# Kernel optimization log

Hardware: AMD Instinct MI355X
Metric: run time of the kernel (lower is better)

The kernel has to match this reference:

```python
import jax, jax.numpy as jnp
import numpy as np

B, T, C, H = 8, 2048, 1024, 16
D = C // H  # head dim


def setup_inputs() -> dict:
    key = jax.random.key(0)
    k1, k2, k3 = jax.random.split(key, 3)
    x = jax.random.normal(k1, (B, T, C), dtype=jnp.float32)
    attention_mask = jnp.ones((B, 1, T), dtype=jnp.int32)
    w_attn = jax.random.normal(k2, (C, 3 * C), dtype=jnp.float32) * 0.02
    b_attn = jnp.zeros((3 * C,), dtype=jnp.float32)
    w_proj = jax.random.normal(k3, (C, C), dtype=jnp.float32) * (0.02 / np.sqrt(2 * 12))
    b_proj = jnp.zeros((C,), dtype=jnp.float32)
    return {"x": x, "attention_mask": attention_mask, "w_attn": w_attn,
            "b_attn": b_attn, "w_proj": w_proj, "b_proj": b_proj}


def reference(x, attention_mask, w_attn, b_attn, w_proj, b_proj):
    Bx, Tx, Cx = x.shape
    qkv = x @ w_attn + b_attn                      # [B,T,3C]
    q, k, v = jnp.split(qkv, 3, axis=2)
    def heads(t):
        return t.reshape(Bx, Tx, H, D).transpose(0, 2, 1, 3)  # [B,H,T,D]
    q, k, v = heads(q), heads(k), heads(v)
    phi_q = jax.nn.elu(q) + 1.0
    phi_k = jax.nn.elu(k) + 1.0
    valid_keys = jnp.any(attention_mask > 0, axis=1).astype(x.dtype)  # [B,T]
    mask = valid_keys[:, None, :, None]            # [B,1,T,1]
    phi_k = phi_k * mask
    v = v * mask
    kv = jnp.einsum('bhtd,bhtf->bhdf', phi_k, v)   # [B,H,D,D]
    k_sum = jnp.sum(phi_k, axis=2, keepdims=True)  # [B,H,1,D]
    numerator = jnp.einsum('bhtd,bhdf->bhtf', phi_q, kv)       # [B,H,T,D]
    denominator = jnp.einsum('bhtd,bhrd->bhtr', phi_q, k_sum)  # [B,H,T,1]
    denominator = jnp.maximum(denominator, 1e-08)
    y = numerator / denominator
    y = y.transpose(0, 2, 1, 3).reshape(Bx, Tx, Cx)
    return y @ w_proj + b_proj
```

## Files before the change

### kernel.cpp

```cpp
#include <hip/hip_runtime.h>

#define Tdim 2048

typedef __attribute__((ext_vector_type(8))) short bf16x8;
typedef __attribute__((ext_vector_type(4))) float f32x4;
typedef __attribute__((ext_vector_type(4))) short short4v;

#define GLOBAL_U32(p) ((const __attribute__((address_space(1))) unsigned int*)(p))
#define LDS_U32(p)    ((__attribute__((address_space(3))) unsigned int*)(p))

#define BARRIER() do { asm volatile("" ::: "memory"); \
                       __builtin_amdgcn_s_barrier(); \
                       asm volatile("" ::: "memory"); } while (0)

__device__ __forceinline__ float phi_f(float x) {
    return x > 0.f ? (x + 1.f) : __expf(x);
}
__device__ __forceinline__ short f2bf(float f) {
    unsigned u = __float_as_uint(f);
    u += 0x7fffu + ((u >> 16) & 1u);
    return (short)(u >> 16);
}
__device__ __forceinline__ float bf2f(short h) {
    return __uint_as_float(((unsigned)(unsigned short)h) << 16);
}


__device__ __forceinline__ void w_tile_body(
    const float* __restrict__ W, int N,
    short* __restrict__ Thi, short* __restrict__ Tlo, int bid)
{
    const int tile = bid * 4 + (threadIdx.x >> 6);
    const int nt = tile >> 5;
    const int kt = tile & 31;
    const int lane = threadIdx.x & 63;
    const int n = nt * 16 + (lane & 15);
    const int k = kt * 32 + (lane >> 4) * 8;
    const float* wp = W + (size_t)k * N + n;
    bf16x8 h, l;
#pragma unroll
    for (int j = 0; j < 8; ++j) {
        const float v = wp[(size_t)j * N];
        const short hh = f2bf(v);
        h[j] = hh;
        l[j] = f2bf(v - bf2f(hh));
    }
    const size_t off = (size_t)tile * 512 + lane * 8;
    *(bf16x8*)(Thi + off) = h;
    *(bf16x8*)(Tlo + off) = l;
}

__global__ __launch_bounds__(256) void prep_kernel(
    const float* __restrict__ X, short* __restrict__ Hi, short* __restrict__ Lo,
    const float* __restrict__ Wa, short* __restrict__ WaHi, short* __restrict__ WaLo,
    const float* __restrict__ Wp, short* __restrict__ WpHi, short* __restrict__ WpLo)
{
    const int bid = blockIdx.x;
    if (bid < 8192) {
        const int rt = bid >> 3;
        const int cb = bid & 7;
        const int t = threadIdx.x;
        const int rl = t >> 4;
        const int cc = t & 15;
        const float* xp = X + ((size_t)rt * 16 + rl) * 1024 + cb * 128 + cc * 8;
        const float4 a = *(const float4*)xp;
        const float4 b = *(const float4*)(xp + 4);
        float v[8] = {a.x, a.y, a.z, a.w, b.x, b.y, b.z, b.w};
        bf16x8 h, l;
#pragma unroll
        for (int j = 0; j < 8; ++j) {
            const short hh = f2bf(v[j]);
            h[j] = hh;
            l[j] = f2bf(v[j] - bf2f(hh));
        }
        const int kt = cb * 4 + (cc >> 2);
        const int slot = ((cc & 3) << 4) | rl;
        const size_t off = ((size_t)rt * 32 + kt) * 512 + slot * 8;
        *(bf16x8*)(Hi + off) = h;
        *(bf16x8*)(Lo + off) = l;
    } else if (bid < 8192 + 1536) {
        w_tile_body(Wa, 3072, WaHi, WaLo, bid - 8192);
    } else {
        w_tile_body(Wp, 1024, WpHi, WpLo, bid - 9728);
    }
}

template<int AMODE>
__global__ __launch_bounds__(512, 2) void gemm3_kernel(
    const short* __restrict__ Ahi, const short* __restrict__ Alo, int lda,
    const short* __restrict__ BThi, const short* __restrict__ BTlo,
    const float* __restrict__ bias, float* __restrict__ C,
    int K, int ldc)
{
    __shared__ short smem[65536];
    const int tid = threadIdx.x;
    const int lane = tid & 63;
    const int wid = tid >> 6;
    const int bx = blockIdx.x, by = blockIdx.y;
    const int wm = wid >> 2, wn = wid & 3;

    const size_t tilestep = (size_t)(K >> 5) * 512;

    const int sel = wid >> 1, half = wid & 1;
    const bool is_a_wave = (wid < 4);
    const short* gptr;
    if (sel >= 2) {
        const short* gb = (sel == 2) ? BThi : BTlo;
        gptr = gb + (size_t)(bx * 16 + half * 8) * tilestep + lane * 8;
    } else if (AMODE == 0) {
        const short* gb = (sel == 0) ? Ahi : Alo;
        gptr = gb + (size_t)(by * 16 + half * 8) * tilestep + lane * 8;
    } else {
        gptr = Ahi + (size_t)((by * 16 + half * 8) * 16) * 6144 + 2048 + lane * 8;
    }
    short* lw = smem + sel * 8192 + half * 4096;

    f32x4 acc[8][4];
#pragma unroll
    for (int i = 0; i < 8; ++i)
#pragma unroll
        for (int j = 0; j < 4; ++j) acc[i][j] = (f32x4){0.f, 0.f, 0.f, 0.f};

    auto stage = [&](int buf, int k0) {
        short* lb = lw + buf * 32768;
        if (AMODE == 0 || sel >= 2) {
            const short* g = gptr + (size_t)(k0 >> 5) * 512;
#pragma unroll
            for (int c = 0; c < 8; ++c)
                __builtin_amdgcn_global_load_lds(
                    GLOBAL_U32(g + (size_t)c * tilestep),
                    LDS_U32(lb + c * 512), 16, 0, 0);
        } else {
            const size_t koff = (size_t)(k0 >> 6) * 6144
                              + (size_t)((((k0 >> 5) & 1) << 1) | sel) * 512;
            const short* g = gptr + koff;
#pragma unroll
            for (int c = 0; c < 8; ++c)
                __builtin_amdgcn_global_load_lds(
                    GLOBAL_U32(g + (size_t)(c * 16) * 6144),
                    LDS_U32(lb + c * 512), 16, 0, 0);
        }
    };

    stage(0, 0);
    __syncthreads();

    const int fo = lane * 8;
    int cur = 0;
    for (int k0 = 0; k0 < K; k0 += 32) {
        const short* bp = smem + cur * 32768;
        const int k0n = (k0 + 32 < K) ? (k0 + 32) : 0;

        if (!is_a_wave) stage(cur ^ 1, k0n);
        bf16x8 bh[4], bl[4];
#pragma unroll
        for (int j = 0; j < 4; ++j) {
            bh[j] = *(const bf16x8*)(bp + 16384 + (wn * 4 + j) * 512 + fo);
            bl[j] = *(const bf16x8*)(bp + 24576 + (wn * 4 + j) * 512 + fo);
        }
        if (is_a_wave) asm volatile("s_waitcnt vmcnt(0)" ::: "memory");
        BARRIER();

        if (is_a_wave) stage(cur ^ 1, k0n);
        __builtin_amdgcn_s_setprio(1);
#pragma unroll
        for (int i = 0; i < 8; ++i) {
            const bf16x8 ah = *(const bf16x8*)(bp + (wm * 8 + i) * 512 + fo);
            const bf16x8 al = *(const bf16x8*)(bp + 8192 + (wm * 8 + i) * 512 + fo);
#pragma unroll
            for (int j = 0; j < 4; ++j) {
                acc[i][j] = __builtin_amdgcn_mfma_f32_16x16x32_bf16(ah, bh[j], acc[i][j], 0, 0, 0);
                acc[i][j] = __builtin_amdgcn_mfma_f32_16x16x32_bf16(al, bh[j], acc[i][j], 0, 0, 0);
                acc[i][j] = __builtin_amdgcn_mfma_f32_16x16x32_bf16(ah, bl[j], acc[i][j], 0, 0, 0);
            }
        }
        __builtin_amdgcn_s_setprio(0);
        if (!is_a_wave) asm volatile("s_waitcnt vmcnt(0)" ::: "memory");
        BARRIER();
        cur ^= 1;
    }

    const int fr = lane & 15, fq = lane >> 4;
#pragma unroll
    for (int i = 0; i < 8; ++i) {
        const size_t row0 = (size_t)by * 256 + wm * 128 + i * 16 + fq * 4;
#pragma unroll
        for (int j = 0; j < 4; ++j) {
            const int col = bx * 256 + wn * 64 + j * 16 + fr;
            const float bv = bias[col];
            float* cp = C + row0 * (size_t)ldc + col;
#pragma unroll
            for (int r = 0; r < 4; ++r)
                cp[(size_t)r * ldc] = acc[i][j][r] + bv;
        }
    }
}

__global__ __launch_bounds__(256) void kv_part_kernel(
    const float* __restrict__ qkv, const int* __restrict__ attn,
    float* __restrict__ kvpart, float* __restrict__ kspart)
{
    __shared__ float ks[32][64];
    __shared__ float vs[32][64];

    const int chunk = blockIdx.x;
    const int bh = blockIdx.y;
    const int b = bh >> 4;
    const int h = bh & 15;
    const int tid = threadIdx.x;
    const int tx = tid & 15;
    const int ty = tid >> 4;
    const int l_t = tid >> 4;
    const int l_d = (tid & 15) << 2;

    const float* kb = qkv + (size_t)b * Tdim * 3072 + 1024 + h * 64;
    const float* vb = qkv + (size_t)b * Tdim * 3072 + 2048 + h * 64;
    const int* am = attn + b * Tdim;

    float acc[4][4];
#pragma unroll
    for (int i = 0; i < 4; ++i)
#pragma unroll
        for (int j = 0; j < 4; ++j) acc[i][j] = 0.f;
    float ksl = 0.f;

    for (int t0 = chunk * 256; t0 < (chunk + 1) * 256; t0 += 32) {
        __syncthreads();
#pragma unroll
        for (int rr = 0; rr < 2; ++rr) {
            const int t = l_t + rr * 16;
            const int gt = t0 + t;
            const float m = (am[gt] > 0) ? 1.f : 0.f;
            const float4 k4 = *(const float4*)(kb + (size_t)gt * 3072 + l_d);
            const float4 v4 = *(const float4*)(vb + (size_t)gt * 3072 + l_d);
            float4 kp, vp;
            kp.x = phi_f(k4.x) * m; kp.y = phi_f(k4.y) * m;
            kp.z = phi_f(k4.z) * m; kp.w = phi_f(k4.w) * m;
            vp.x = v4.x * m; vp.y = v4.y * m; vp.z = v4.z * m; vp.w = v4.w * m;
            *(float4*)&ks[t][l_d] = kp;
            *(float4*)&vs[t][l_d] = vp;
        }
        __syncthreads();
#pragma unroll
        for (int t = 0; t < 32; ++t) {
            float kr[4], vr[4];
            *(float4*)kr = *(const float4*)&ks[t][ty * 4];
            *(float4*)vr = *(const float4*)&vs[t][tx * 4];
#pragma unroll
            for (int i = 0; i < 4; ++i)
#pragma unroll
                for (int j = 0; j < 4; ++j)
                    acc[i][j] = fmaf(kr[i], vr[j], acc[i][j]);
        }
        if (tid < 64) {
#pragma unroll
            for (int t = 0; t < 32; ++t) ksl += ks[t][tid];
        }
    }

    float* ko = kvpart + ((size_t)bh * 8 + chunk) * 4096;
#pragma unroll
    for (int i = 0; i < 4; ++i) {
        float4 o;
        o.x = acc[i][0]; o.y = acc[i][1]; o.z = acc[i][2]; o.w = acc[i][3];
        *(float4*)(ko + (ty * 4 + i) * 64 + tx * 4) = o;
    }
    if (tid < 64) kspart[((size_t)bh * 8 + chunk) * 64 + tid] = ksl;
}

__global__ __launch_bounds__(256) void kv_reduce_kernel(
    const float* __restrict__ kvpart, const float* __restrict__ kspart,
    short* __restrict__ kvT, float* __restrict__ ksum)
{
    __shared__ float kvs[64][68];
    const int bh = blockIdx.x;
    const int tid = threadIdx.x;
    const float4* p = (const float4*)(kvpart + (size_t)bh * 8 * 4096);
    float4 s0 = {0,0,0,0}, s1 = {0,0,0,0}, s2 = {0,0,0,0}, s3 = {0,0,0,0};
#pragma unroll
    for (int c = 0; c < 8; ++c) {
        const int base = c * 1024;
        float4 a = p[base + tid], b = p[base + 256 + tid],
               cc = p[base + 512 + tid], d = p[base + 768 + tid];
        s0.x += a.x; s0.y += a.y; s0.z += a.z; s0.w += a.w;
        s1.x += b.x; s1.y += b.y; s1.z += b.z; s1.w += b.w;
        s2.x += cc.x; s2.y += cc.y; s2.z += cc.z; s2.w += cc.w;
        s3.x += d.x; s3.y += d.y; s3.z += d.z; s3.w += d.w;
    }
    const int d0 = tid >> 4, f0 = (tid & 15) * 4;
    *(float4*)&kvs[d0 +  0][f0] = s0;
    *(float4*)&kvs[d0 + 16][f0] = s1;
    *(float4*)&kvs[d0 + 32][f0] = s2;
    *(float4*)&kvs[d0 + 48][f0] = s3;
    __syncthreads();

    short* kvb = kvT + (size_t)bh * 8192;
#pragma unroll
    for (int pp = 0; pp < 2; ++pp) {
        const int sid = tid * 2 + pp;
        const int tt = sid >> 6;
        const int L = sid & 63;
        const int nt = tt >> 1, kt = tt & 1;
        const int f = nt * 16 + (L & 15);
        const int dd = kt * 32 + (L >> 4) * 8;
        bf16x8 h, l;
#pragma unroll
        for (int e = 0; e < 8; ++e) {
            const float v = kvs[dd + e][f];
            const short hh = f2bf(v);
            h[e] = hh;
            l[e] = f2bf(v - bf2f(hh));
        }
        *(bf16x8*)(kvb + tt * 512 + L * 8) = h;
        *(bf16x8*)(kvb + 4096 + tt * 512 + L * 8) = l;
    }
    if (tid < 64) {
        float ss = 0.f;
#pragma unroll
        for (int c = 0; c < 8; ++c) ss += kspart[((size_t)bh * 8 + c) * 64 + tid];
        ksum[bh * 64 + tid] = ss;
    }
}

__global__ __launch_bounds__(256) void attn_y_kernel(
    float* __restrict__ qkv, const short* __restrict__ kvT,
    const float* __restrict__ ksumin)
{
    __shared__ short kvs[8192];
    __shared__ float den_s[4][16];

    const int bh = blockIdx.y;
    const int b = bh >> 4;
    const int hh = bh & 15;
    const int t0 = blockIdx.x * 64;
    const int tid = threadIdx.x;
    const int lane = tid & 63;
    const int wid = tid >> 6;

    {
        const short* src = kvT + (size_t)bh * 8192 + (wid * 4) * 512 + lane * 8;
        short* dst = kvs + (wid * 4) * 512;
#pragma unroll
        for (int t = 0; t < 4; ++t)
            __builtin_amdgcn_global_load_lds(
                GLOBAL_U32(src + t * 512), LDS_U32(dst + t * 512), 16, 0, 0);
    }

    const int grow = b * Tdim + t0 + wid * 16 + (lane & 15);
    const int kc = (lane >> 4) * 8;
    const float* qp = qkv + (size_t)grow * 3072 + hh * 64 + kc;
    const float* kp = ksumin + bh * 64 + kc;
    bf16x8 qh[2], ql[2];
    float den = 0.f;
#pragma unroll
    for (int ks = 0; ks < 2; ++ks) {
        const float4 a = *(const float4*)(qp + ks * 32);
        const float4 c = *(const float4*)(qp + ks * 32 + 4);
        const float4 u = *(const float4*)(kp + ks * 32);
        const float4 w = *(const float4*)(kp + ks * 32 + 4);
        float qv[8] = {a.x, a.y, a.z, a.w, c.x, c.y, c.z, c.w};
        float sv[8] = {u.x, u.y, u.z, u.w, w.x, w.y, w.z, w.w};
#pragma unroll
        for (int e = 0; e < 8; ++e) {
            const float ph = phi_f(qv[e]);
            den = fmaf(ph, sv[e], den);
            const short hi = f2bf(ph);
            qh[ks][e] = hi;
            ql[ks][e] = f2bf(ph - bf2f(hi));
        }
    }
    den += __shfl_xor(den, 16);
    den += __shfl_xor(den, 32);
    if ((lane >> 4) == 0) den_s[wid][lane & 15] = den;
    __syncthreads();

    f32x4 acc[4];
#pragma unroll
    for (int j = 0; j < 4; ++j) acc[j] = (f32x4){0.f, 0.f, 0.f, 0.f};
#pragma unroll
    for (int j = 0; j < 4; ++j) {
#pragma unroll
        for (int ks = 0; ks < 2; ++ks) {
            const short* tb = kvs + (j * 2 + ks) * 512 + lane * 8;
            const bf16x8 ahf = *(const bf16x8*)tb;
            const bf16x8 alf = *(const bf16x8*)(tb + 4096);
            acc[j] = __builtin_amdgcn_mfma_f32_16x16x32_bf16(ahf, qh[ks], acc[j], 0, 0, 0);
            acc[j] = __builtin_amdgcn_mfma_f32_16x16x32_bf16(alf, qh[ks], acc[j], 0, 0, 0);
            acc[j] = __builtin_amdgcn_mfma_f32_16x16x32_bf16(ahf, ql[ks], acc[j], 0, 0, 0);
        }
    }

    const float dinv = 1.f / fmaxf(den_s[wid][lane & 15], 1e-8f);

    short* yb = (short*)qkv;
    const int RT = ((b * Tdim + t0) >> 4) + wid;
    const size_t rowbase = (size_t)(RT * 16 + hh) * 6144 + 2048;
    const int fq = lane >> 4;
    const int trow = lane & 15;
#pragma unroll
    for (int j = 0; j < 4; ++j) {
        short4v hv, lv;
#pragma unroll
        for (int r = 0; r < 4; ++r) {
            const float val = acc[j][r] * dinv;
            const short h = f2bf(val);
            hv[r] = h;
            lv[r] = f2bf(val - bf2f(h));
        }
        const int fbase = j * 16 + fq * 4;
        const int kl = fbase >> 5;
        const int cc = (fbase & 31) >> 3;
        const int wi = fbase & 7;
        const size_t so = rowbase + (size_t)(kl * 2) * 512
                        + (size_t)((cc << 4) | trow) * 8 + wi;
        *(short4v*)(yb + so) = hv;
        *(short4v*)(yb + so + 512) = lv;
    }
}

extern "C" void kernel_launch(void* const* d_in, const int* in_sizes, int n_in,
                              void* d_out, int out_size, void* d_ws, size_t ws_size,
                              hipStream_t stream)
{
    const float* x      = (const float*)d_in[0];
    const int*   attn   = (const int*)  d_in[1];
    const float* w_attn = (const float*)d_in[2];
    const float* b_attn = (const float*)d_in[3];
    const float* w_proj = (const float*)d_in[4];
    const float* b_proj = (const float*)d_in[5];
    float* out = (float*)d_out;

    char* ws = (char*)d_ws;
    size_t off = 0;
    auto alloc = [&](size_t bytes) { void* p = ws + off; off = (off + bytes + 255) & ~(size_t)255; return p; };
    float* qkv   = (float*)alloc((size_t)16384 * 3072 * 4);
    short* waThi = (short*)alloc((size_t)3072 * 1024 * 2);
    short* waTlo = (short*)alloc((size_t)3072 * 1024 * 2);
    short* wpThi = (short*)alloc((size_t)1024 * 1024 * 2);
    short* wpTlo = (short*)alloc((size_t)1024 * 1024 * 2);
    short* kvbT  = (short*)alloc((size_t)128 * 8192 * 2);
    float* ksum  = (float*)alloc((size_t)128 * 64 * 4);

    short* xhi = (short*)d_out;
    short* xlo = xhi + (size_t)16384 * 1024;
    float* kvpart = (float*)d_out;
    float* kspart = (float*)((char*)d_out + (size_t)128 * 8 * 4096 * 4);

    prep_kernel<<<10240, 256, 0, stream>>>(x, xhi, xlo,
                                           w_attn, waThi, waTlo,
                                           w_proj, wpThi, wpTlo);
    gemm3_kernel<0><<<dim3(12, 64), 512, 0, stream>>>(xhi, xlo, 0, waThi, waTlo, b_attn, qkv, 1024, 3072);
    kv_part_kernel<<<dim3(8, 128), 256, 0, stream>>>(qkv, attn, kvpart, kspart);
    kv_reduce_kernel<<<128, 256, 0, stream>>>(kvpart, kspart, kvbT, ksum);
    attn_y_kernel<<<dim3(32, 128), 256, 0, stream>>>(qkv, kvbT, ksum);
    gemm3_kernel<2><<<dim3(4, 64), 512, 0, stream>>>((const short*)qkv, (const short*)qkv, 0,
                                                     wpThi, wpTlo, b_proj, out, 1024, 1024);
}
```

Measured before the change: 553.8 us.

## Fuse phi/mask/bf16 split into QKV GEMM epilogue and compute KV with MFMA

The QKV GEMM epilogue now applies phi and the attention mask to K and V and writes them directly as hi/lo bf16 tiles in an MFMA-ready transposed layout. Only Q is stored as fp32. The scalar-FMA kv_part kernel is replaced by an MFMA kernel that computes K^T V and the k-sums (via a ones operand) over four chunks, and a reduce/emit kernel combines them. Y is written in tiled hi/lo form into the reused V buffer and feeds the projection GEMM. This removes the fp32 K/V round trip and the scalar FMA work, at the cost of more complex epilogue stores and extra workspace.

```diff
diff --git a/kernel.cpp b/kernel.cpp
--- a/kernel.cpp
+++ b/kernel.cpp
@@ -85,12 +85,15 @@
     }
 }
 
-template<int AMODE>
+template<int MODE>
 __global__ __launch_bounds__(512, 2) void gemm3_kernel(
-    const short* __restrict__ Ahi, const short* __restrict__ Alo, int lda,
+    const short* __restrict__ Ahi, const short* __restrict__ Alo,
     const short* __restrict__ BThi, const short* __restrict__ BTlo,
     const float* __restrict__ bias, float* __restrict__ C,
-    int K, int ldc)
+    int K, int ldc,
+    short* __restrict__ KThi, short* __restrict__ KTlo,
+    short* __restrict__ VThi, short* __restrict__ VTlo,
+    const int* __restrict__ attn)
 {
     __shared__ short smem[65536];
     const int tid = threadIdx.x;
@@ -107,11 +110,9 @@
     if (sel >= 2) {
         const short* gb = (sel == 2) ? BThi : BTlo;
         gptr = gb + (size_t)(bx * 16 + half * 8) * tilestep + lane * 8;
-    } else if (AMODE == 0) {
+    } else {
         const short* gb = (sel == 0) ? Ahi : Alo;
         gptr = gb + (size_t)(by * 16 + half * 8) * tilestep + lane * 8;
-    } else {
-        gptr = Ahi + (size_t)((by * 16 + half * 8) * 16) * 6144 + 2048 + lane * 8;
     }
     short* lw = smem + sel * 8192 + half * 4096;
 
@@ -123,23 +124,12 @@
 
     auto stage = [&](int buf, int k0) {
         short* lb = lw + buf * 32768;
-        if (AMODE == 0 || sel >= 2) {
-            const short* g = gptr + (size_t)(k0 >> 5) * 512;
-#pragma unroll
-            for (int c = 0; c < 8; ++c)
-                __builtin_amdgcn_global_load_lds(
-                    GLOBAL_U32(g + (size_t)c * tilestep),
-                    LDS_U32(lb + c * 512), 16, 0, 0);
-        } else {
-            const size_t koff = (size_t)(k0 >> 6) * 6144
-                              + (size_t)((((k0 >> 5) & 1) << 1) | sel) * 512;
-            const short* g = gptr + koff;
-#pragma unroll
-            for (int c = 0; c < 8; ++c)
-                __builtin_amdgcn_global_load_lds(
-                    GLOBAL_U32(g + (size_t)(c * 16) * 6144),
-                    LDS_U32(lb + c * 512), 16, 0, 0);
-        }
+        const short* g = gptr + (size_t)(k0 >> 5) * 512;
+#pragma unroll
+        for (int c = 0; c < 8; ++c)
+            __builtin_amdgcn_global_load_lds(
+                GLOBAL_U32(g + (size_t)c * tilestep),
+                LDS_U32(lb + c * 512), 16, 0, 0);
     };
 
     stage(0, 0);
@@ -181,117 +171,162 @@
     }
 
     const int fr = lane & 15, fq = lane >> 4;
-#pragma unroll
-    for (int i = 0; i < 8; ++i) {
-        const size_t row0 = (size_t)by * 256 + wm * 128 + i * 16 + fq * 4;
-#pragma unroll
-        for (int j = 0; j < 4; ++j) {
-            const int col = bx * 256 + wn * 64 + j * 16 + fr;
-            const float bv = bias[col];
-            float* cp = C + row0 * (size_t)ldc + col;
-#pragma unroll
-            for (int r = 0; r < 4; ++r)
-                cp[(size_t)r * ldc] = acc[i][j][r] + bv;
-        }
-    }
-}
-
-__global__ __launch_bounds__(256) void kv_part_kernel(
-    const float* __restrict__ qkv, const int* __restrict__ attn,
+    const int sec = (MODE == 1) ? (bx >> 2) : 0;
+
+    if (MODE == 0 || sec == 0) {
+#pragma unroll
+        for (int i = 0; i < 8; ++i) {
+            const size_t row0 = (size_t)by * 256 + wm * 128 + i * 16 + fq * 4;
+#pragma unroll
+            for (int j = 0; j < 4; ++j) {
+                const int col = bx * 256 + wn * 64 + j * 16 + fr;
+                const float bv = bias[col];
+                float* cp = C + row0 * (size_t)ldc + col;
+#pragma unroll
+                for (int r = 0; r < 4; ++r)
+                    cp[(size_t)r * ldc] = acc[i][j][r] + bv;
+            }
+        }
+    } else {
+        const int b = by >> 3;
+        const int head = (bx - (sec == 1 ? 4 : 8)) * 4 + wn;
+        const int bh = b * 16 + head;
+        short* Phi = (sec == 1) ? KThi : VThi;
+        short* Plo = (sec == 1) ? KTlo : VTlo;
+        const size_t base = (size_t)bh * 131072;
+        const int e0 = (fq & 1) * 4;
+#pragma unroll
+        for (int i = 0; i < 8; ++i) {
+            const int row0 = by * 256 + wm * 128 + i * 16 + fq * 4;
+            const int t = row0 & 2047;
+            const int kt = t >> 5;
+            const int Lrow = ((t >> 3) & 3) << 4;
+            const int4 ap = *(const int4*)(attn + row0);
+            const int mm[4] = {ap.x, ap.y, ap.z, ap.w};
+#pragma unroll
+            for (int j = 0; j < 4; ++j) {
+                const int col = bx * 256 + wn * 64 + j * 16 + fr;
+                const float bv = bias[col];
+                short4v hv, lv;
+#pragma unroll
+                for (int r = 0; r < 4; ++r) {
+                    float val = acc[i][j][r] + bv;
+                    if (sec == 1) val = phi_f(val);
+                    val = (mm[r] > 0) ? val : 0.f;
+                    const short h = f2bf(val);
+                    hv[r] = h;
+                    lv[r] = f2bf(val - bf2f(h));
+                }
+                const size_t addr = base + (size_t)(j * 64 + kt) * 512
+                                  + (size_t)(Lrow | fr) * 8 + e0;
+                *(short4v*)(Phi + addr) = hv;
+                *(short4v*)(Plo + addr) = lv;
+            }
+        }
+    }
+}
+
+__global__ __launch_bounds__(256) void kv_mfma_kernel(
+    const short* __restrict__ KThi, const short* __restrict__ KTlo,
+    const short* __restrict__ VThi, const short* __restrict__ VTlo,
     float* __restrict__ kvpart, float* __restrict__ kspart)
 {
-    __shared__ float ks[32][64];
-    __shared__ float vs[32][64];
-
-    const int chunk = blockIdx.x;
+    __shared__ short smem[2][16][512];
+    __shared__ float kvs2[64][68];
+    const int c = blockIdx.x;
     const int bh = blockIdx.y;
-    const int b = bh >> 4;
-    const int h = bh & 15;
     const int tid = threadIdx.x;
-    const int tx = tid & 15;
-    const int ty = tid >> 4;
-    const int l_t = tid >> 4;
-    const int l_d = (tid & 15) << 2;
-
-    const float* kb = qkv + (size_t)b * Tdim * 3072 + 1024 + h * 64;
-    const float* vb = qkv + (size_t)b * Tdim * 3072 + 2048 + h * 64;
-    const int* am = attn + b * Tdim;
-
-    float acc[4][4];
-#pragma unroll
-    for (int i = 0; i < 4; ++i)
-#pragma unroll
-        for (int j = 0; j < 4; ++j) acc[i][j] = 0.f;
-    float ksl = 0.f;
-
-    for (int t0 = chunk * 256; t0 < (chunk + 1) * 256; t0 += 32) {
+    const int lane = tid & 63;
+    const int w = tid >> 6;
+
+    const size_t base = (size_t)bh * 131072 + (size_t)(w * 64) * 512 + lane * 8;
+    const short* va = VThi + base;
+    const short* vl = VTlo + base;
+    const short* ka = KThi + base;
+    const short* kl = KTlo + base;
+
+    f32x4 acc[4];
+#pragma unroll
+    for (int rd = 0; rd < 4; ++rd) acc[rd] = (f32x4){0.f, 0.f, 0.f, 0.f};
+    f32x4 ksa = (f32x4){0.f, 0.f, 0.f, 0.f};
+    bf16x8 ones;
+#pragma unroll
+    for (int e = 0; e < 8; ++e) ones[e] = (short)0x3F80;
+
+    auto stage = [&](int buf, int kt) {
+        __builtin_amdgcn_global_load_lds(GLOBAL_U32(va + (size_t)kt * 512),
+                                         LDS_U32(&smem[buf][w][0]), 16, 0, 0);
+        __builtin_amdgcn_global_load_lds(GLOBAL_U32(vl + (size_t)kt * 512),
+                                         LDS_U32(&smem[buf][4 + w][0]), 16, 0, 0);
+        __builtin_amdgcn_global_load_lds(GLOBAL_U32(ka + (size_t)kt * 512),
+                                         LDS_U32(&smem[buf][8 + w][0]), 16, 0, 0);
+        __builtin_amdgcn_global_load_lds(GLOBAL_U32(kl + (size_t)kt * 512),
+                                         LDS_U32(&smem[buf][12 + w][0]), 16, 0, 0);
+    };
+
+    stage(0, c * 16);
+    __syncthreads();
+    int cur = 0;
+    for (int s = 0; s < 16; ++s) {
+        if (s + 1 < 16) stage(cur ^ 1, c * 16 + s + 1);
+        const short* bp = &smem[cur][0][0];
+        const bf16x8 ah = *(const bf16x8*)(bp + w * 512 + lane * 8);
+        const bf16x8 al = *(const bf16x8*)(bp + (4 + w) * 512 + lane * 8);
+#pragma unroll
+        for (int rd = 0; rd < 4; ++rd) {
+            const bf16x8 bhf = *(const bf16x8*)(bp + (8 + rd) * 512 + lane * 8);
+            const bf16x8 blf = *(const bf16x8*)(bp + (12 + rd) * 512 + lane * 8);
+            acc[rd] = __builtin_amdgcn_mfma_f32_16x16x32_bf16(ah, bhf, acc[rd], 0, 0, 0);
+            acc[rd] = __builtin_amdgcn_mfma_f32_16x16x32_bf16(al, bhf, acc[rd], 0, 0, 0);
+            acc[rd] = __builtin_amdgcn_mfma_f32_16x16x32_bf16(ah, blf, acc[rd], 0, 0, 0);
+            if (rd == w) {
+                ksa = __builtin_amdgcn_mfma_f32_16x16x32_bf16(ones, bhf, ksa, 0, 0, 0);
+                ksa = __builtin_amdgcn_mfma_f32_16x16x32_bf16(ones, blf, ksa, 0, 0, 0);
+            }
+        }
         __syncthreads();
-#pragma unroll
-        for (int rr = 0; rr < 2; ++rr) {
-            const int t = l_t + rr * 16;
-            const int gt = t0 + t;
-            const float m = (am[gt] > 0) ? 1.f : 0.f;
-            const float4 k4 = *(const float4*)(kb + (size_t)gt * 3072 + l_d);
-            const float4 v4 = *(const float4*)(vb + (size_t)gt * 3072 + l_d);
-            float4 kp, vp;
-            kp.x = phi_f(k4.x) * m; kp.y = phi_f(k4.y) * m;
-            kp.z = phi_f(k4.z) * m; kp.w = phi_f(k4.w) * m;
-            vp.x = v4.x * m; vp.y = v4.y * m; vp.z = v4.z * m; vp.w = v4.w * m;
-            *(float4*)&ks[t][l_d] = kp;
-            *(float4*)&vs[t][l_d] = vp;
-        }
-        __syncthreads();
-#pragma unroll
-        for (int t = 0; t < 32; ++t) {
-            float kr[4], vr[4];
-            *(float4*)kr = *(const float4*)&ks[t][ty * 4];
-            *(float4*)vr = *(const float4*)&vs[t][tx * 4];
-#pragma unroll
-            for (int i = 0; i < 4; ++i)
-#pragma unroll
-                for (int j = 0; j < 4; ++j)
-                    acc[i][j] = fmaf(kr[i], vr[j], acc[i][j]);
-        }
-        if (tid < 64) {
-#pragma unroll
-            for (int t = 0; t < 32; ++t) ksl += ks[t][tid];
-        }
-    }
-
-    float* ko = kvpart + ((size_t)bh * 8 + chunk) * 4096;
+        cur ^= 1;
+    }
+
+    const int fr = lane & 15, fq = lane >> 4;
+#pragma unroll
+    for (int rd = 0; rd < 4; ++rd)
+#pragma unroll
+        for (int r = 0; r < 4; ++r)
+            kvs2[w * 16 + fq * 4 + r][rd * 16 + fr] = acc[rd][r];
+    if (lane < 16)
+        kspart[((size_t)c * 128 + bh) * 64 + w * 16 + lane] = ksa[0];
+    __syncthreads();
+
+    float* kp = kvpart + ((size_t)c * 128 + bh) * 4096;
 #pragma unroll
     for (int i = 0; i < 4; ++i) {
-        float4 o;
-        o.x = acc[i][0]; o.y = acc[i][1]; o.z = acc[i][2]; o.w = acc[i][3];
-        *(float4*)(ko + (ty * 4 + i) * 64 + tx * 4) = o;
-    }
-    if (tid < 64) kspart[((size_t)bh * 8 + chunk) * 64 + tid] = ksl;
-}
-
-__global__ __launch_bounds__(256) void kv_reduce_kernel(
+        const int idx = i * 256 + tid;
+        const int f = idx >> 4, d0 = (idx & 15) * 4;
+        *(float4*)(kp + f * 64 + d0) = *(const float4*)&kvs2[f][d0];
+    }
+}
+
+__global__ __launch_bounds__(256) void kv_emit_kernel(
     const float* __restrict__ kvpart, const float* __restrict__ kspart,
     short* __restrict__ kvT, float* __restrict__ ksum)
 {
-    __shared__ float kvs[64][68];
+    __shared__ float kvsE[64][68];
     const int bh = blockIdx.x;
     const int tid = threadIdx.x;
-    const float4* p = (const float4*)(kvpart + (size_t)bh * 8 * 4096);
-    float4 s0 = {0,0,0,0}, s1 = {0,0,0,0}, s2 = {0,0,0,0}, s3 = {0,0,0,0};
-#pragma unroll
-    for (int c = 0; c < 8; ++c) {
-        const int base = c * 1024;
-        float4 a = p[base + tid], b = p[base + 256 + tid],
-               cc = p[base + 512 + tid], d = p[base + 768 + tid];
-        s0.x += a.x; s0.y += a.y; s0.z += a.z; s0.w += a.w;
-        s1.x += b.x; s1.y += b.y; s1.z += b.z; s1.w += b.w;
-        s2.x += cc.x; s2.y += cc.y; s2.z += cc.z; s2.w += cc.w;
-        s3.x += d.x; s3.y += d.y; s3.z += d.z; s3.w += d.w;
-    }
-    const int d0 = tid >> 4, f0 = (tid & 15) * 4;
-    *(float4*)&kvs[d0 +  0][f0] = s0;
-    *(float4*)&kvs[d0 + 16][f0] = s1;
-    *(float4*)&kvs[d0 + 32][f0] = s2;
-    *(float4*)&kvs[d0 + 48][f0] = s3;
+#pragma unroll
+    for (int i = 0; i < 4; ++i) {
+        const int idx = i * 256 + tid;
+        const int f = idx >> 4, d0 = (idx & 15) * 4;
+        float4 s = {0.f, 0.f, 0.f, 0.f};
+#pragma unroll
+        for (int c = 0; c < 4; ++c) {
+            const float4 p = *(const float4*)(kvpart
+                + ((size_t)c * 128 + bh) * 4096 + f * 64 + d0);
+            s.x += p.x; s.y += p.y; s.z += p.z; s.w += p.w;
+        }
+        *(float4*)&kvsE[f][d0] = s;
+    }
     __syncthreads();
 
     short* kvb = kvT + (size_t)bh * 8192;
@@ -306,7 +341,7 @@
         bf16x8 h, l;
 #pragma unroll
         for (int e = 0; e < 8; ++e) {
-            const float v = kvs[dd + e][f];
+            const float v = kvsE[f][dd + e];
             const short hh = f2bf(v);
             h[e] = hh;
             l[e] = f2bf(v - bf2f(hh));
@@ -317,14 +352,16 @@
     if (tid < 64) {
         float ss = 0.f;
 #pragma unroll
-        for (int c = 0; c < 8; ++c) ss += kspart[((size_t)bh * 8 + c) * 64 + tid];
+        for (int c = 0; c < 4; ++c)
+            ss += kspart[((size_t)c * 128 + bh) * 64 + tid];
         ksum[bh * 64 + tid] = ss;
     }
 }
 
 __global__ __launch_bounds__(256) void attn_y_kernel(
-    float* __restrict__ qkv, const short* __restrict__ kvT,
-    const float* __restrict__ ksumin)
+    const float* __restrict__ Q, const short* __restrict__ kvT,
+    const float* __restrict__ ksumin,
+    short* __restrict__ Yhi, short* __restrict__ Ylo)
 {
     __shared__ short kvs[8192];
     __shared__ float den_s[4][16];
@@ -348,7 +385,7 @@
 
     const int grow = b * Tdim + t0 + wid * 16 + (lane & 15);
     const int kc = (lane >> 4) * 8;
-    const float* qp = qkv + (size_t)grow * 3072 + hh * 64 + kc;
+    const float* qp = Q + (size_t)grow * 1024 + hh * 64 + kc;
     const float* kp = ksumin + bh * 64 + kc;
     bf16x8 qh[2], ql[2];
     float den = 0.f;
@@ -392,11 +429,11 @@
 
     const float dinv = 1.f / fmaxf(den_s[wid][lane & 15], 1e-8f);
 
-    short* yb = (short*)qkv;
-    const int RT = ((b * Tdim + t0) >> 4) + wid;
-    const size_t rowbase = (size_t)(RT * 16 + hh) * 6144 + 2048;
     const int fq = lane >> 4;
     const int trow = lane & 15;
+    const int tg = b * Tdim + t0 + wid * 16 + trow;
+    const int RT = tg >> 4;
+    const int e0 = (fq & 1) * 4;
 #pragma unroll
     for (int j = 0; j < 4; ++j) {
         short4v hv, lv;
@@ -407,14 +444,12 @@
             hv[r] = h;
             lv[r] = f2bf(val - bf2f(h));
         }
-        const int fbase = j * 16 + fq * 4;
-        const int kl = fbase >> 5;
-        const int cc = (fbase & 31) >> 3;
-        const int wi = fbase & 7;
-        const size_t so = rowbase + (size_t)(kl * 2) * 512
-                        + (size_t)((cc << 4) | trow) * 8 + wi;
-        *(short4v*)(yb + so) = hv;
-        *(short4v*)(yb + so + 512) = lv;
+        const int col = hh * 64 + j * 16 + fq * 4;
+        const int ktc = col >> 5;
+        const int L = (((col >> 3) & 3) << 4) | trow;
+        const size_t addr = (size_t)(RT * 32 + ktc) * 512 + (size_t)L * 8 + e0;
+        *(short4v*)(Yhi + addr) = hv;
+        *(short4v*)(Ylo + addr) = lv;
     }
 }
 
@@ -433,7 +468,11 @@
     char* ws = (char*)d_ws;
     size_t off = 0;
     auto alloc = [&](size_t bytes) { void* p = ws + off; off = (off + bytes + 255) & ~(size_t)255; return p; };
-    float* qkv   = (float*)alloc((size_t)16384 * 3072 * 4);
+    float* Q     = (float*)alloc((size_t)16384 * 1024 * 4);
+    short* KThi  = (short*)alloc((size_t)128 * 131072 * 2);
+    short* KTlo  = (short*)alloc((size_t)128 * 131072 * 2);
+    short* VThi  = (short*)alloc((size_t)128 * 131072 * 2);
+    short* VTlo  = (short*)alloc((size_t)128 * 131072 * 2);
     short* waThi = (short*)alloc((size_t)3072 * 1024 * 2);
     short* waTlo = (short*)alloc((size_t)3072 * 1024 * 2);
     short* wpThi = (short*)alloc((size_t)1024 * 1024 * 2);
@@ -444,15 +483,19 @@
     short* xhi = (short*)d_out;
     short* xlo = xhi + (size_t)16384 * 1024;
     float* kvpart = (float*)d_out;
-    float* kspart = (float*)((char*)d_out + (size_t)128 * 8 * 4096 * 4);
+    float* kspart = (float*)((char*)d_out + (size_t)4 * 128 * 4096 * 4);
 
     prep_kernel<<<10240, 256, 0, stream>>>(x, xhi, xlo,
                                            w_attn, waThi, waTlo,
                                            w_proj, wpThi, wpTlo);
-    gemm3_kernel<0><<<dim3(12, 64), 512, 0, stream>>>(xhi, xlo, 0, waThi, waTlo, b_attn, qkv, 1024, 3072);
-    kv_part_kernel<<<dim3(8, 128), 256, 0, stream>>>(qkv, attn, kvpart, kspart);
-    kv_reduce_kernel<<<128, 256, 0, stream>>>(kvpart, kspart, kvbT, ksum);
-    attn_y_kernel<<<dim3(32, 128), 256, 0, stream>>>(qkv, kvbT, ksum);
-    gemm3_kernel<2><<<dim3(4, 64), 512, 0, stream>>>((const short*)qkv, (const short*)qkv, 0,
-                                                     wpThi, wpTlo, b_proj, out, 1024, 1024);
-}
+    gemm3_kernel<1><<<dim3(12, 64), 512, 0, stream>>>(
+        xhi, xlo, waThi, waTlo, b_attn, Q, 1024, 1024,
+        KThi, KTlo, VThi, VTlo, attn);
+    kv_mfma_kernel<<<dim3(4, 128), 256, 0, stream>>>(KThi, KTlo, VThi, VTlo,
+                                                     kvpart, kspart);
+    kv_emit_kernel<<<128, 256, 0, stream>>>(kvpart, kspart, kvbT, ksum);
+    attn_y_kernel<<<dim3(32, 128), 256, 0, stream>>>(Q, kvbT, ksum, VThi, VTlo);
+    gemm3_kernel<0><<<dim3(4, 64), 512, 0, stream>>>(
+        VThi, VTlo, wpThi, wpTlo, b_proj, out, 1024, 1024,
+        nullptr, nullptr, nullptr, nullptr, nullptr);
+}
```

New measurement: 513.6 us. 1.08x faster.
